# Kernel tuning notes

Measured on AMD Instinct MI355X. Metric: run time of the kernel, lower is better.

Reference implementation:

```python
import jax, jax.numpy as jnp
import numpy as np


def _mab(Q, K, wq, bq, wk, bk, wv, bv, wo, bo, num_heads):
    # Faithful MAB (no LayerNorm: ln=False throughout SetPooler's settrans).
    V = wq.shape[1]
    dh = V // num_heads
    q = Q @ wq + bq          # [..., Sq, V]
    k = K @ wk + bk          # [..., Sk, V]
    v = K @ wv + bv
    def heads(x):
        return x.reshape(*x.shape[:-1], num_heads, dh).swapaxes(-2, -3)  # [..., h, S, dh]
    qh, kh, vh = heads(q), heads(k), heads(v)
    scale = jnp.asarray(1.0 / np.sqrt(V), q.dtype)  # note: torch code scales by sqrt(dim_V), not sqrt(head_dim)
    A = jax.nn.softmax(jnp.einsum('...hqd,...hkd->...hqk', qh, kh) * scale, axis=-1)
    O = qh + jnp.einsum('...hqk,...hkd->...hqd', A, vh)               # residual on Q_
    O = O.swapaxes(-2, -3).reshape(*Q.shape[:-1], V)                  # merge heads back
    return O + jax.nn.relu(O @ wo + bo)


def _forward(rep_R, GA,
             sab0_wq, sab0_bq, sab0_wk, sab0_bk, sab0_wv, sab0_bv, sab0_wo, sab0_bo,
             sab1_wq, sab1_bq, sab1_wk, sab1_bk, sab1_wv, sab1_bv, sab1_wo, sab1_bo,
             pma_S, pma_wq, pma_bq, pma_wk, pma_bk, pma_wv, pma_bv, pma_wo, pma_bo,
             mlp_w1, mlp_b1, mlp_w2, mlp_b2, mlp_w3, mlp_b3):
    # masked mul: GA [G,N] -> [1,G,N,1] broadcast against rep_R [B,G,N,D]
    X = GA[None, :, :, None] * rep_R
    # two SABs (self-attention), 4 heads each
    X = _mab(X, X, sab0_wq, sab0_bq, sab0_wk, sab0_bk, sab0_wv, sab0_bv, sab0_wo, sab0_bo, 4)
    X = _mab(X, X, sab1_wq, sab1_bq, sab1_wk, sab1_bk, sab1_wv, sab1_bv, sab1_wo, sab1_bo, 4)
    # PMA: 1 learned seed, 2 heads, squeeze_out
    S = jnp.broadcast_to(pma_S, (*X.shape[:-2], *pma_S.shape))  # [B,G,1,D]
    O = _mab(S, X, pma_wq, pma_bq, pma_wk, pma_bk, pma_wv, pma_bv, pma_wo, pma_bo, 2)
    O = O[..., 0, :]  # squeeze_out -> [B,G,D]
    # MLP head: D -> 512 -> 512 -> 2*dim_z
    h = jax.nn.relu(O @ mlp_w1 + mlp_b1)
    h = jax.nn.relu(h @ mlp_w2 + mlp_b2)
    return h @ mlp_w3 + mlp_b3


def setup_inputs() -> dict:
    key = jax.random.key(0)
    B, G, N, D = 4, 16, 512, 256
    dz2 = 256  # 2 * dim_z
    ks = iter(jax.random.split(key, 64))
    def lin(fi, fo):
        w = jax.random.normal(next(ks), (fi, fo), jnp.float32) / np.float32(np.sqrt(fi))
        return w, jnp.zeros((fo,), jnp.float32)
    inp = {}
    inp['rep_R'] = jax.random.normal(next(ks), (B, G, N, D), jnp.float32)
    inp['GA'] = jax.random.uniform(next(ks), (G, N), jnp.float32)
    for i in range(2):
        for nm in ('q', 'k', 'v', 'o'):
            w, b = lin(D, D)
            inp[f'sab{i}_w{nm}'] = w
            inp[f'sab{i}_b{nm}'] = b
    inp['pma_S'] = jax.random.normal(next(ks), (1, D), jnp.float32) * np.float32(np.sqrt(6.0 / (1 + D)))
    for nm in ('q', 'k', 'v', 'o'):
        w, b = lin(D, D)
        inp[f'pma_w{nm}'] = w
        inp[f'pma_b{nm}'] = b
    inp['mlp_w1'], inp['mlp_b1'] = lin(D, 512)
    inp['mlp_w2'], inp['mlp_b2'] = lin(512, 512)
    inp['mlp_w3'], inp['mlp_b3'] = lin(512, dz2)
    return inp


def reference(rep_R, GA,
              sab0_wq, sab0_bq, sab0_wk, sab0_bk, sab0_wv, sab0_bv, sab0_wo, sab0_bo,
              sab1_wq, sab1_bq, sab1_wk, sab1_bk, sab1_wv, sab1_bv, sab1_wo, sab1_bo,
              pma_S, pma_wq, pma_bq, pma_wk, pma_bk, pma_wv, pma_bv, pma_wo, pma_bo,
              mlp_w1, mlp_b1, mlp_w2, mlp_b2, mlp_w3, mlp_b3):
    return _forward(rep_R, GA,
                    sab0_wq, sab0_bq, sab0_wk, sab0_bk, sab0_wv, sab0_bv, sab0_wo, sab0_bo,
                    sab1_wq, sab1_bq, sab1_wk, sab1_bk, sab1_wv, sab1_bv, sab1_wo, sab1_bo,
                    pma_S, pma_wq, pma_bq, pma_wk, pma_bk, pma_wv, pma_bv, pma_wo, pma_bo,
                    mlp_w1, mlp_b1, mlp_w2, mlp_b2, mlp_w3, mlp_b3)
```

## Files before the change

kernel.cpp:

```cpp
#include <hip/hip_runtime.h>
#include <hip/hip_bf16.h>

typedef __attribute__((ext_vector_type(4)))  float  f32x4;
typedef __attribute__((ext_vector_type(8)))  __bf16 bf16x8;
typedef __attribute__((ext_vector_type(4)))  __bf16 bf16x4;

#define LOG2E_O16 0.09016844005556021f

__device__ __forceinline__ void gload_lds16(const void* g, void* l) {
  __builtin_amdgcn_global_load_lds(
      (const __attribute__((address_space(1))) void*)g,
      (__attribute__((address_space(3))) void*)l, 16, 0, 0);
}

__global__ __launch_bounds__(256) void scale_kernel(
    const float* __restrict__ rep, const float* __restrict__ GA, __bf16* __restrict__ X)
{
  size_t i = (size_t)blockIdx.x * 256 + threadIdx.x;
  size_t e = i * 4;
  f32x4 r = *(const f32x4*)(rep + e);
  int dn = (int)(e >> 8);
  int n  = dn & 511;
  int g  = (dn >> 9) & 15;
  float ga = GA[g * 512 + n];
  bf16x4 o;
  o[0] = (__bf16)(r[0] * ga); o[1] = (__bf16)(r[1] * ga);
  o[2] = (__bf16)(r[2] * ga); o[3] = (__bf16)(r[3] * ga);
  *(bf16x4*)(X + e) = o;
}

struct WPtrs { const float* w[10]; };
__global__ __launch_bounds__(256) void wconv_kernel(WPtrs ws, __bf16* __restrict__ out)
{
  __shared__ float t[64][65];
  const float* w = ws.w[blockIdx.y];
  __bf16* o = out + (size_t)blockIdx.y * 65536;
  const int tr = (blockIdx.x & 3) * 64, tc = (blockIdx.x >> 2) * 64;
  const int r4 = threadIdx.x >> 6, c = threadIdx.x & 63;
#pragma unroll
  for (int p = 0; p < 16; ++p) {
    int row = p * 4 + r4;
    t[row][c] = w[(size_t)(tr + row) * 256 + tc + c];
  }
  __syncthreads();
#pragma unroll
  for (int p = 0; p < 16; ++p) {
    int row = p * 4 + r4;
    o[(size_t)(tc + row) * 256 + tr + c] = (__bf16)t[c][row];
  }
}

#define STAGE_T(A_, B_, bmv, bnv, Kv, tt, bb) do {                                 \
    _Pragma("unroll")                                                              \
    for (int r = 0; r < 4; ++r) {                                                  \
      int rowl = r * 32 + (tid >> 3);                                              \
      int sl = (tid & 7) ^ (rowl & 7);                                             \
      gload_lds16((const char*)((A_) + (size_t)((bmv) + rowl) * (Kv) + (tt) * 64) + sl * 16, \
                  (char*)sA + (bb) * 16384 + r * 4096 + wv * 1024);                \
      gload_lds16((const char*)((B_) + (size_t)((bnv) + rowl) * (Kv) + (tt) * 64) + sl * 16, \
                  (char*)sB + (bb) * 16384 + r * 4096 + wv * 1024);                \
    } } while (0)

#define GEMM64_PIPE(A_, B_, bmv, bnv, Kv)                                          \
  f32x4 acc[4][4] = {};                                                            \
  const int nt = (Kv) >> 6;                                                        \
  STAGE_T(A_, B_, bmv, bnv, Kv, 0, 0);                                             \
  asm volatile("s_waitcnt vmcnt(0)" ::: "memory");                                 \
  __builtin_amdgcn_s_barrier();                                                    \
  for (int t = 0; t < nt; ++t) {                                                   \
    if (t + 1 < nt) STAGE_T(A_, B_, bmv, bnv, Kv, t + 1, (t + 1) & 1);             \
    const char* bA = (const char*)sA + (t & 1) * 16384;                            \
    const char* bB = (const char*)sB + (t & 1) * 16384;                            \
    bf16x8 af[4][2], bfr[4][2];                                                    \
    _Pragma("unroll")                                                              \
    for (int mi = 0; mi < 4; ++mi) {                                               \
      int row = wr + mi * 16 + l16;                                                \
      _Pragma("unroll")                                                            \
      for (int kk = 0; kk < 2; ++kk) {                                             \
        int sl = (kk * 4 + lg) ^ (row & 7);                                        \
        af[mi][kk] = *(const bf16x8*)(bA + row * 128 + sl * 16);                   \
      }                                                                            \
    }                                                                              \
    _Pragma("unroll")                                                              \
    for (int ni = 0; ni < 4; ++ni) {                                               \
      int row = wc + ni * 16 + l16;                                                \
      _Pragma("unroll")                                                            \
      for (int kk = 0; kk < 2; ++kk) {                                             \
        int sl = (kk * 4 + lg) ^ (row & 7);                                        \
        bfr[ni][kk] = *(const bf16x8*)(bB + row * 128 + sl * 16);                  \
      }                                                                            \
    }                                                                              \
    _Pragma("unroll")                                                              \
    for (int kk = 0; kk < 2; ++kk)                                                 \
      _Pragma("unroll")                                                            \
      for (int mi = 0; mi < 4; ++mi)                                               \
        _Pragma("unroll")                                                          \
        for (int ni = 0; ni < 4; ++ni)                                             \
          acc[mi][ni] = __builtin_amdgcn_mfma_f32_16x16x32_bf16(                   \
              af[mi][kk], bfr[ni][kk], acc[mi][ni], 0, 0, 0);                      \
    asm volatile("s_waitcnt vmcnt(0)" ::: "memory");                               \
    __builtin_amdgcn_s_barrier();                                                  \
  }

struct QKV3 {
  const __bf16* Bt[3];
  const float* bias[3];
  __bf16* out[3];
};

template<int NW>
__global__ __launch_bounds__(256) void gemmqkv_kernel(
    const __bf16* __restrict__ A, QKV3 args, int K)
{
  __shared__ __align__(16) __bf16 smem[32768];
  __bf16* const sA = smem;
  __bf16* const sB = smem + 16384;
  __bf16* const sC = smem;
  const int tid = threadIdx.x, lane = tid & 63, wv = tid >> 6;
  const int l16 = lane & 15, lg = lane >> 4;
  const int wr = (wv >> 1) * 64, wc = (wv & 1) * 64;

  const int nblk = gridDim.x, cpx = nblk >> 3, orig = blockIdx.x;
  const int wg  = (orig & 7) * cpx + (orig >> 3);
  const int r_  = wg / (2 * NW), rem = wg % (2 * NW);
  const int j   = rem >> 1;
  const int bm  = r_ * 128, bn = (rem & 1) * 128;
  const __bf16* __restrict__ Bt = args.Bt[j];

  GEMM64_PIPE(A, Bt, bm, bn, K)

  const float* bias = args.bias[j];
  __bf16* C = args.out[j];
#pragma unroll
  for (int mi = 0; mi < 4; ++mi)
#pragma unroll
    for (int ni = 0; ni < 4; ++ni) {
      int cl = wc + ni * 16 + l16;
      float bval = bias[bn + cl];
      int r0 = wr + mi * 16 + lg * 4;
#pragma unroll
      for (int i = 0; i < 4; ++i)
        sC[(r0 + i) * 136 + cl] = (__bf16)(acc[mi][ni][i] + bval);
    }
  __syncthreads();
#pragma unroll
  for (int it = 0; it < 8; ++it) {
    int idx = it * 256 + tid;
    int r = idx >> 4, seg = idx & 15;
    bf16x8 cv = *(const bf16x8*)&sC[r * 136 + seg * 8];
    *(bf16x8*)(C + (size_t)(bm + r) * 256 + bn + seg * 8) = cv;
  }
}

__global__ __launch_bounds__(256) void gemm128_kernel(
    const __bf16* __restrict__ A, const __bf16* __restrict__ Bt,
    const float* __restrict__ bias, const __bf16* __restrict__ R,
    __bf16* __restrict__ C, int K)
{
  __shared__ __align__(16) __bf16 smem[32768];
  __bf16* const sA = smem;
  __bf16* const sB = smem + 16384;
  __bf16* const sC = smem;
  const int tid = threadIdx.x, lane = tid & 63, wv = tid >> 6;
  const int l16 = lane & 15, lg = lane >> 4;
  const int wr = (wv >> 1) * 64, wc = (wv & 1) * 64;

  const int nblk = gridDim.x, cpx = nblk >> 3, orig = blockIdx.x;
  const int wg  = (orig & 7) * cpx + (orig >> 3);
  const int bm  = (wg >> 1) * 128, bn = (wg & 1) * 128;

  GEMM64_PIPE(A, Bt, bm, bn, K)

  const float* __restrict__ biasp = bias;
#pragma unroll
  for (int mi = 0; mi < 4; ++mi)
#pragma unroll
    for (int ni = 0; ni < 4; ++ni) {
      int cl = wc + ni * 16 + l16;
      float bval = biasp[bn + cl];
      int r0 = wr + mi * 16 + lg * 4;
#pragma unroll
      for (int i = 0; i < 4; ++i)
        sC[(r0 + i) * 136 + cl] = (__bf16)fmaxf(acc[mi][ni][i] + bval, 0.f);
    }
  __syncthreads();
#pragma unroll
  for (int it = 0; it < 8; ++it) {
    int idx = it * 256 + tid;
    int r = idx >> 4, seg = idx & 15;
    bf16x8 cv = *(const bf16x8*)&sC[r * 136 + seg * 8];
    bf16x8 rv = *(const bf16x8*)(R + (size_t)(bm + r) * 256 + bn + seg * 8);
    bf16x8 ov;
#pragma unroll
    for (int i = 0; i < 8; ++i)
      ov[i] = (__bf16)((float)rv[i] + (float)cv[i]);
    *(bf16x8*)(C + (size_t)(bm + r) * 256 + bn + seg * 8) = ov;
  }
}

template<int EPI, bool OUTF32>
__global__ __launch_bounds__(256) void gemm_kernel(
    const __bf16* __restrict__ A, const float* __restrict__ B,
    const float* __restrict__ bias, const __bf16* __restrict__ R,
    void* __restrict__ Cv, int M, int N, int K)
{
  __shared__ __bf16 sA[64][40];
  __shared__ __bf16 sB[64][40];
  const int tid  = threadIdx.x;
  const int lane = tid & 63;
  const int wv   = tid >> 6;
  const int wr   = (wv >> 1) * 32;
  const int wc   = (wv & 1) * 32;
  const int bm   = blockIdx.x * 64;
  const int bn   = blockIdx.y * 64;
  const int l16  = lane & 15;
  const int lk8  = (lane >> 4) * 8;

  const int a_r = tid >> 2, a_c = (tid & 3) * 8;
  const int b_c = tid & 63, b_k = (tid >> 6) * 8;

  f32x4 acc[2][2] = {};

  for (int k0 = 0; k0 < K; k0 += 32) {
    bf16x8 av = *(const bf16x8*)(A + (size_t)(bm + a_r) * K + k0 + a_c);
    float bvf[8];
#pragma unroll
    for (int j = 0; j < 8; ++j)
      bvf[j] = B[(size_t)(k0 + b_k + j) * N + bn + b_c];
    *(bf16x8*)&sA[a_r][a_c] = av;
    bf16x8 bb;
#pragma unroll
    for (int j = 0; j < 8; ++j) bb[j] = (__bf16)bvf[j];
    *(bf16x8*)&sB[b_c][b_k] = bb;
    __syncthreads();
    bf16x8 af0 = *(const bf16x8*)&sA[wr + l16][lk8];
    bf16x8 af1 = *(const bf16x8*)&sA[wr + 16 + l16][lk8];
    bf16x8 bf0 = *(const bf16x8*)&sB[wc + l16][lk8];
    bf16x8 bf1 = *(const bf16x8*)&sB[wc + 16 + l16][lk8];
    acc[0][0] = __builtin_amdgcn_mfma_f32_16x16x32_bf16(af0, bf0, acc[0][0], 0, 0, 0);
    acc[0][1] = __builtin_amdgcn_mfma_f32_16x16x32_bf16(af0, bf1, acc[0][1], 0, 0, 0);
    acc[1][0] = __builtin_amdgcn_mfma_f32_16x16x32_bf16(af1, bf0, acc[1][0], 0, 0, 0);
    acc[1][1] = __builtin_amdgcn_mfma_f32_16x16x32_bf16(af1, bf1, acc[1][1], 0, 0, 0);
    __syncthreads();
  }

#pragma unroll
  for (int mi = 0; mi < 2; ++mi)
#pragma unroll
    for (int ni = 0; ni < 2; ++ni) {
      int col = bn + wc + ni * 16 + l16;
      float bval = bias[col];
      int row0 = bm + wr + mi * 16 + (lane >> 4) * 4;
#pragma unroll
      for (int i = 0; i < 4; ++i) {
        int row = row0 + i;
        float v = acc[mi][ni][i] + bval;
        if (EPI == 1) v = fmaxf(v, 0.f);
        if (EPI == 2) v = (float)R[(size_t)row * N + col] + fmaxf(v, 0.f);
        if (OUTF32) ((float*)Cv)[(size_t)row * N + col] = v;
        else        ((__bf16*)Cv)[(size_t)row * N + col] = (__bf16)v;
      }
    }
}

__global__ __launch_bounds__(512, 2) void attn_sab_kernel(
    __bf16* __restrict__ Q, const __bf16* __restrict__ Kb, const __bf16* __restrict__ Vb)
{
  __shared__ __align__(16) __bf16 sK[128][72];
  __shared__ __align__(16) __bf16 sV[64][136];
  __shared__ __align__(16) __bf16 sP[8][16][72];

  const int orig = blockIdx.x;
  const int wg   = (orig & 7) * 64 + (orig >> 3);
  const int qh   = wg & 1;
  const int pair = wg >> 1;
  const int head = pair & 3;
  const int item = pair >> 2;

  const int tid  = threadIdx.x;
  const int lane = tid & 63;
  const int wv   = tid >> 6;
  const int l16  = lane & 15;
  const int lg   = lane >> 4;
  const size_t base = (size_t)item * (512 * 256) + (size_t)head * 64;
  const int qrow0 = qh * 256 + wv * 32;

  bf16x8 aq[2][2];
#pragma unroll
  for (int qb = 0; qb < 2; ++qb) {
    const size_t qrow = base + (size_t)(qrow0 + qb * 16 + l16) * 256;
    aq[qb][0] = *(const bf16x8*)(Q + qrow + lg * 8);
    aq[qb][1] = *(const bf16x8*)(Q + qrow + 32 + lg * 8);
  }

  f32x4 acco[2][4] = {};
  float lsum[2] = {0.f, 0.f};

  const int kr  = tid >> 3, kc8 = (tid & 7) * 8;
  const int vch = tid & 63, vk8 = (tid >> 6) * 8;

  bf16x8 kreg[2], vreg[2];

#define LOADC(cc) do {                                                             \
    _Pragma("unroll")                                                              \
    for (int p = 0; p < 2; ++p) {                                                  \
      kreg[p] = *(const bf16x8*)(Kb + base + (size_t)((cc)*128 + p*64 + kr)*256 + kc8); \
      bf16x8 vv;                                                                   \
      _Pragma("unroll")                                                            \
      for (int jj = 0; jj < 8; ++jj)                                               \
        vv[jj] = Vb[base + (size_t)((cc)*128 + p*64 + vk8 + jj)*256 + vch];        \
      vreg[p] = vv;                                                                \
    } } while (0)

  LOADC(0);

  for (int c = 0; c < 4; ++c) {
    if (c) __syncthreads();
#pragma unroll
    for (int p = 0; p < 2; ++p) {
      *(bf16x8*)&sK[p * 64 + kr][kc8] = kreg[p];
      *(bf16x8*)&sV[vch][p * 64 + vk8] = vreg[p];
    }
    __syncthreads();
    if (c < 3) LOADC(c + 1);

#pragma unroll
    for (int half = 0; half < 2; ++half) {
      bf16x8 kf0[4], kf1[4];
#pragma unroll
      for (int st = 0; st < 4; ++st) {
        int krl = half * 64 + st * 16 + l16;
        kf0[st] = *(const bf16x8*)&sK[krl][lg * 8];
        kf1[st] = *(const bf16x8*)&sK[krl][32 + lg * 8];
      }
      bf16x8 vf[2][4];
#pragma unroll
      for (int kk = 0; kk < 2; ++kk)
#pragma unroll
        for (int vt = 0; vt < 4; ++vt)
          vf[kk][vt] = *(const bf16x8*)&sV[vt * 16 + l16][half * 64 + kk * 32 + lg * 8];

#pragma unroll
      for (int qb = 0; qb < 2; ++qb) {
        f32x4 s[4];
#pragma unroll
        for (int st = 0; st < 4; ++st) {
          f32x4 z = {};
          s[st] = __builtin_amdgcn_mfma_f32_16x16x32_bf16(kf0[st], aq[qb][0], z, 0, 0, 0);
        }
#pragma unroll
        for (int st = 0; st < 4; ++st)
          s[st] = __builtin_amdgcn_mfma_f32_16x16x32_bf16(kf1[st], aq[qb][1], s[st], 0, 0, 0);
#pragma unroll
        for (int st = 0; st < 4; ++st) {
          bf16x4 pv4;
          float ls = 0.f;
#pragma unroll
          for (int i = 0; i < 4; ++i) {
            float p = __builtin_amdgcn_exp2f(s[st][i] * LOG2E_O16);
            ls += p;
            pv4[i] = (__bf16)p;
          }
          lsum[qb] += ls;
          *(bf16x4*)&sP[wv][l16][st * 16 + lg * 4] = pv4;
        }
#pragma unroll
        for (int kk = 0; kk < 2; ++kk) {
          bf16x8 ap = *(const bf16x8*)&sP[wv][l16][kk * 32 + lg * 8];
#pragma unroll
          for (int vt = 0; vt < 4; ++vt)
            acco[qb][vt] = __builtin_amdgcn_mfma_f32_16x16x32_bf16(ap, vf[kk][vt], acco[qb][vt], 0, 0, 0);
        }
      }
    }
  }
#undef LOADC

#pragma unroll
  for (int qb = 0; qb < 2; ++qb) {
    float t = lsum[qb];
    t += __shfl_xor(t, 16, 64);
    t += __shfl_xor(t, 32, 64);
#pragma unroll
    for (int i = 0; i < 4; ++i) {
      float tot = __shfl(t, lg * 4 + i, 64);
      float inv = 1.0f / tot;
      int row = qrow0 + qb * 16 + lg * 4 + i;
#pragma unroll
      for (int vt = 0; vt < 4; ++vt) {
        size_t idx = base + (size_t)row * 256 + vt * 16 + l16;
        Q[idx] = (__bf16)((float)Q[idx] + acco[qb][vt][i] * inv);
      }
    }
  }
}

__global__ __launch_bounds__(256) void pma_attn_kernel(
    const float* __restrict__ S, const float* __restrict__ wq,
    const float* __restrict__ bq, const __bf16* __restrict__ Kb,
    const __bf16* __restrict__ Vb, __bf16* __restrict__ Opma)
{
  __shared__ float sS[256];
  __shared__ float sq[256];
  __shared__ float sP[1024];
  __shared__ float red[256];
  __shared__ float sl[2];
  const int item = blockIdx.x;
  const int t = threadIdx.x;
  sS[t] = S[t];
  __syncthreads();
  {
    float acc = bq[t];
#pragma unroll 8
    for (int k = 0; k < 256; ++k) acc += sS[k] * wq[k * 256 + t];
    sq[t] = acc;
  }
  __syncthreads();

#pragma unroll
  for (int rep = 0; rep < 4; ++rep) {
    int task = rep * 256 + t;
    int h = task >> 9, key = task & 511;
    const __bf16* kr = Kb + ((size_t)item * 512 + key) * 256 + h * 128;
    float s = 0.f;
#pragma unroll
    for (int d8 = 0; d8 < 128; d8 += 8) {
      bf16x8 kv = *(const bf16x8*)(kr + d8);
#pragma unroll
      for (int j = 0; j < 8; ++j) s += sq[h * 128 + d8 + j] * (float)kv[j];
    }
    sP[task] = __builtin_amdgcn_exp2f(s * LOG2E_O16);
  }
  __syncthreads();
  {
    int h = t >> 7, kb = t & 127;
    float p = 0.f;
#pragma unroll
    for (int j = 0; j < 4; ++j) p += sP[h * 512 + kb + j * 128];
    red[t] = p;
  }
  __syncthreads();
  if (t < 2) {
    float s = 0.f;
    for (int i = 0; i < 128; ++i) s += red[t * 128 + i];
    sl[t] = 1.f / s;
  }
  __syncthreads();
  {
    int h = t >> 7;
    float acc = 0.f;
    for (int key = 0; key < 512; ++key)
      acc += sP[h * 512 + key] * (float)Vb[((size_t)item * 512 + key) * 256 + t];
    Opma[item * 256 + t] = (__bf16)(sq[t] + acc * sl[h]);
  }
}

extern "C" void kernel_launch(void* const* d_in, const int* in_sizes, int n_in,
                              void* d_out, int out_size, void* d_ws, size_t ws_size,
                              hipStream_t stream)
{
  const size_t XSZ = (size_t)64 * 512 * 256;
  if (ws_size < 4 * XSZ * sizeof(__bf16) + (4u << 20)) return;

  const float* rep = (const float*)d_in[0];
  const float* GA  = (const float*)d_in[1];

  __bf16* X    = (__bf16*)d_ws;
  __bf16* Qb   = X  + XSZ;
  __bf16* Kb   = Qb + XSZ;
  __bf16* Vb   = Kb + XSZ;
  __bf16* wT   = Vb + XSZ;
  __bf16* Opma = wT + 10 * 65536;
  __bf16* O2   = Opma + 64 * 256;
  __bf16* H1   = O2 + 64 * 256;
  __bf16* H2   = H1 + 64 * 512;

  WPtrs wp;
  for (int s = 0; s < 2; ++s)
    for (int j = 0; j < 4; ++j)
      wp.w[s * 4 + j] = (const float*)d_in[2 + s * 8 + j * 2];
  wp.w[8] = (const float*)d_in[21];
  wp.w[9] = (const float*)d_in[23];
  wconv_kernel<<<dim3(16, 10), 256, 0, stream>>>(wp, wT);

  scale_kernel<<<8192, 256, 0, stream>>>(rep, GA, X);

  for (int sab = 0; sab < 2; ++sab) {
    QKV3 a;
    a.Bt[0] = wT + (size_t)(sab * 4 + 0) * 65536;
    a.Bt[1] = wT + (size_t)(sab * 4 + 1) * 65536;
    a.Bt[2] = wT + (size_t)(sab * 4 + 2) * 65536;
    a.bias[0] = (const float*)d_in[2 + sab * 8 + 1];
    a.bias[1] = (const float*)d_in[2 + sab * 8 + 3];
    a.bias[2] = (const float*)d_in[2 + sab * 8 + 5];
    a.out[0] = Qb; a.out[1] = Kb; a.out[2] = Vb;
    gemmqkv_kernel<3><<<1536, 256, 0, stream>>>(X, a, 256);
    attn_sab_kernel<<<512, 512, 0, stream>>>(Qb, Kb, Vb);
    gemm128_kernel<<<512, 256, 0, stream>>>(Qb, wT + (size_t)(sab * 4 + 3) * 65536,
        (const float*)d_in[2 + sab * 8 + 7], Qb, X, 256);
  }

  {
    QKV3 a;
    a.Bt[0] = wT + (size_t)8 * 65536;
    a.Bt[1] = wT + (size_t)9 * 65536;
    a.Bt[2] = wT;
    a.bias[0] = (const float*)d_in[22];
    a.bias[1] = (const float*)d_in[24];
    a.bias[2] = (const float*)d_in[22];
    a.out[0] = Kb; a.out[1] = Vb; a.out[2] = Kb;
    gemmqkv_kernel<2><<<1024, 256, 0, stream>>>(X, a, 256);
  }
  pma_attn_kernel<<<64, 256, 0, stream>>>((const float*)d_in[18], (const float*)d_in[19],
      (const float*)d_in[20], Kb, Vb, Opma);
  gemm_kernel<2, false><<<dim3(1, 4), 256, 0, stream>>>(Opma, (const float*)d_in[25],
      (const float*)d_in[26], Opma, O2, 64, 256, 256);
  gemm_kernel<1, false><<<dim3(1, 8), 256, 0, stream>>>(O2, (const float*)d_in[27],
      (const float*)d_in[28], nullptr, H1, 64, 512, 256);
  gemm_kernel<1, false><<<dim3(1, 8), 256, 0, stream>>>(H1, (const float*)d_in[29],
      (const float*)d_in[30], nullptr, H2, 64, 512, 512);
  gemm_kernel<0, true><<<dim3(1, 4), 256, 0, stream>>>(H2, (const float*)d_in[31],
      (const float*)d_in[32], nullptr, (float*)d_out, 64, 256, 512);
}
```

Measured before the change: 223.5 us.

## Split PMA attention across four blocks per item with wave-shuffle softmax sum

The PMA attention kernel now launches four blocks per set item, each handling one head and a 64-channel quarter of the output. Inside a block the P·V product is split by key segments across waves and then reduced through shared memory. The softmax denominator is computed with wave shuffles in place of a serial two-thread loop. This raises parallelism from 64 blocks to 256 and shortens the serial reduction, but each block recomputes the seed query projection and the score pass, so that work is done redundantly.

```diff
diff --git a/kernel.cpp b/kernel.cpp
--- a/kernel.cpp
+++ b/kernel.cpp
@@ -402,11 +402,17 @@
 {
   __shared__ float sS[256];
   __shared__ float sq[256];
-  __shared__ float sP[1024];
+  __shared__ float sP[512];
+  __shared__ float wsum[4];
+  __shared__ float sl0;
   __shared__ float red[256];
-  __shared__ float sl[2];
-  const int item = blockIdx.x;
+
+  const int item = blockIdx.x >> 2;
+  const int quarter = blockIdx.x & 3;
+  const int h = quarter >> 1;
   const int t = threadIdx.x;
+  const int lane = t & 63, wv = t >> 6;
+
   sS[t] = S[t];
   __syncthreads();
   {
@@ -418,9 +424,8 @@
   __syncthreads();
 
 #pragma unroll
-  for (int rep = 0; rep < 4; ++rep) {
-    int task = rep * 256 + t;
-    int h = task >> 9, key = task & 511;
+  for (int rep = 0; rep < 2; ++rep) {
+    int key = rep * 256 + t;
     const __bf16* kr = Kb + ((size_t)item * 512 + key) * 256 + h * 128;
     float s = 0.f;
 #pragma unroll
@@ -429,29 +434,34 @@
 #pragma unroll
       for (int j = 0; j < 8; ++j) s += sq[h * 128 + d8 + j] * (float)kv[j];
     }
-    sP[task] = __builtin_amdgcn_exp2f(s * LOG2E_O16);
-  }
-  __syncthreads();
+    sP[key] = __builtin_amdgcn_exp2f(s * LOG2E_O16);
+  }
+  __syncthreads();
+
   {
-    int h = t >> 7, kb = t & 127;
-    float p = 0.f;
-#pragma unroll
-    for (int j = 0; j < 4; ++j) p += sP[h * 512 + kb + j * 128];
-    red[t] = p;
-  }
-  __syncthreads();
-  if (t < 2) {
-    float s = 0.f;
-    for (int i = 0; i < 128; ++i) s += red[t * 128 + i];
-    sl[t] = 1.f / s;
-  }
-  __syncthreads();
+    float p = sP[t] + sP[t + 256];
+#pragma unroll
+    for (int m = 1; m < 64; m <<= 1) p += __shfl_xor(p, m, 64);
+    if (lane == 0) wsum[wv] = p;
+  }
+  __syncthreads();
+  if (t == 0) sl0 = 1.0f / (wsum[0] + wsum[1] + wsum[2] + wsum[3]);
+
   {
-    int h = t >> 7;
+    const int chl = t & 63, seg = t >> 6;
+    const int ch = quarter * 64 + chl;
+    const __bf16* vp = Vb + ((size_t)item * 512 + seg * 128) * 256 + ch;
     float acc = 0.f;
-    for (int key = 0; key < 512; ++key)
-      acc += sP[h * 512 + key] * (float)Vb[((size_t)item * 512 + key) * 256 + t];
-    Opma[item * 256 + t] = (__bf16)(sq[t] + acc * sl[h]);
+#pragma unroll 4
+    for (int k = 0; k < 128; ++k)
+      acc += sP[seg * 128 + k] * (float)vp[(size_t)k * 256];
+    red[t] = acc;
+  }
+  __syncthreads();
+  if (t < 64) {
+    int ch = quarter * 64 + t;
+    float a = red[t] + red[t + 64] + red[t + 128] + red[t + 192];
+    Opma[item * 256 + ch] = (__bf16)(sq[ch] + a * sl0);
   }
 }
 
@@ -511,7 +521,7 @@
     a.out[0] = Kb; a.out[1] = Vb; a.out[2] = Kb;
     gemmqkv_kernel<2><<<1024, 256, 0, stream>>>(X, a, 256);
   }
-  pma_attn_kernel<<<64, 256, 0, stream>>>((const float*)d_in[18], (const float*)d_in[19],
+  pma_attn_kernel<<<256, 256, 0, stream>>>((const float*)d_in[18], (const float*)d_in[19],
       (const float*)d_in[20], Kb, Vb, Opma);
   gemm_kernel<2, false><<<dim3(1, 4), 256, 0, stream>>>(Opma, (const float*)d_in[25],
       (const float*)d_in[26], Opma, O2, 64, 256, 256);
```

New measurement: 218.7 us (median of 2 runs). -2.1%, faster.
